# Kernel optimization log

Hardware: AMD Instinct MI355X
Metric: run time of the kernel (lower is better)

## Reference

```python
import jax, jax.numpy as jnp
import numpy as np

CIN = 128
COUT = 128
B = 8192
N_DIAG = 17
LENS = [9 - abs(i - 8) for i in range(N_DIAG)]  # [1,2,...,9,...,2,1]


def setup_inputs() -> dict:
    key = jax.random.key(0)
    ks = jax.random.split(key, 2 + N_DIAG)
    d = {
        "weights": jax.random.normal(ks[0], (N_DIAG, COUT, CIN), jnp.float32),
        "bias": jax.random.normal(ks[1], (N_DIAG, COUT), jnp.float32),
    }
    for i, L in enumerate(LENS):
        d[f"x{i}"] = jax.random.normal(ks[2 + i], (B, L, CIN), jnp.float32)
    return d


def _diag_idx(i):
    # board positions (r, c) on anti-diagonal r + c == i of a 9x9 board
    rs = np.arange(max(0, i - 8), min(8, i) + 1)
    cs = i - rs
    return rs, cs


def _forward(weights, bias, xs):
    b = xs[0].shape[0]
    out = jnp.zeros((b, 9, 9, weights.shape[1]), xs[0].dtype)
    for i, x in enumerate(xs):
        # per-diagonal linear transform: (B, L_i, Cin) @ (Cout, Cin)^T + bias
        y = jnp.einsum('blc,oc->blo', x, weights[i]) + bias[i]
        rs, cs = _diag_idx(i)  # static numpy indices -> jit-friendly scatter
        out = out.at[:, rs, cs, :].set(y)
    return out


def reference(weights, bias, x0, x1, x2, x3, x4, x5, x6, x7, x8, x9, x10, x11,
              x12, x13, x14, x15, x16):
    xs = (x0, x1, x2, x3, x4, x5, x6, x7, x8, x9, x10, x11, x12, x13, x14,
          x15, x16)
    return _forward(weights, bias, xs)
```

## Files before the change

kernel.cpp:

```cpp
#include <hip/hip_runtime.h>
#include <hip/hip_bf16.h>

typedef __attribute__((ext_vector_type(8))) short short8;
typedef __attribute__((ext_vector_type(4))) float f32x4;
typedef __attribute__((ext_vector_type(4))) unsigned int u32x4;

struct XPtrs { const float* p[17]; };
struct Bases { int v[18]; };

#define CPB 5

__device__ __forceinline__ unsigned short f2bf(float f) {
  unsigned u = __float_as_uint(f);
  return (unsigned short)((u + 0x7fffu + ((u >> 16) & 1u)) >> 16);
}

__global__ __launch_bounds__(1024) void convert_w_kernel(
    const float* __restrict__ W, unsigned short* __restrict__ ws) {
  const int tid = blockIdx.x * 1024 + threadIdx.x;
  const int d  = tid >> 11;
  const int s2 = tid & 2047;
  const int sg = s2 >> 7;
  const int n  = s2 & 127;
  const float* src = W + ((size_t)d * 128 + n) * 128 + sg * 8;
  float4 a = *(const float4*)(src);
  float4 b = *(const float4*)(src + 4);
  unsigned u0 = (unsigned)f2bf(a.x) | ((unsigned)f2bf(a.y) << 16);
  unsigned u1 = (unsigned)f2bf(a.z) | ((unsigned)f2bf(a.w) << 16);
  unsigned u2 = (unsigned)f2bf(b.x) | ((unsigned)f2bf(b.y) << 16);
  unsigned u3 = (unsigned)f2bf(b.z) | ((unsigned)f2bf(b.w) << 16);
  *(uint4*)(ws + (size_t)tid * 8) = make_uint4(u0, u1, u2, u3);
}

__device__ __forceinline__ unsigned pack_bf2(float lo, float hi) {
  unsigned rl = __float_as_uint(lo) + 0x8000u;
  unsigned rh = __float_as_uint(hi) + 0x8000u;
  return __builtin_amdgcn_perm(rh, rl, 0x07060302u);
}

__global__ __launch_bounds__(256) void diag_linear_kernel(
    XPtrs xp, Bases bb, const unsigned short* __restrict__ wsrc,
    const float* __restrict__ bias, float* __restrict__ out) {
  const int bid = blockIdx.x;
  int d = 0;
#pragma unroll
  for (int i = 1; i < 17; ++i) d += (bid >= bb.v[i]) ? 1 : 0;
  const int L = 9 - ((d < 8) ? (8 - d) : (d - 8));
  const int start = (d > 8) ? (d - 8) : 0;
  const float* __restrict__ x = xp.p[d];
  const int nunits = 128 * L;
  const int u0 = (bid - bb.v[d]) * CPB;
  const int nit = min(CPB, nunits - u0);

  const int t = threadIdx.x;
  const int lane = t & 63;
  const int wave = t >> 6;
  const int lr = lane & 15;
  const int lg = lane >> 4;

  __shared__ unsigned short wlds[2048 * 8];
  __shared__ float blds[128];

  {
    const unsigned short* gw = wsrc + (size_t)d * 16384;
    typedef const __attribute__((address_space(1))) unsigned int* gas_u32;
    typedef __attribute__((address_space(3))) unsigned int* las_u32;
#pragma unroll
    for (int r = 0; r < 8; ++r) {
      const int slotbase = (wave * 8 + r) * 64;
      __builtin_amdgcn_global_load_lds(
          (gas_u32)(const void*)(gw + (size_t)(slotbase + lane) * 8),
          (las_u32)(void*)(wlds + (size_t)slotbase * 8),
          16, 0, 0);
    }
    if (t < 32) {
      __builtin_amdgcn_global_load_lds(
          (gas_u32)(const void*)(bias + d * 128 + t * 4),
          (las_u32)(void*)(blds), 16, 0, 0);
    }
  }

  float4 pf[8];
  {
    const float* xr = x + ((size_t)(u0 * 64 + wave * 16 + lr)) * 128 + lg * 8;
#pragma unroll
    for (int s = 0; s < 4; ++s) {
      pf[2 * s]     = *(const float4*)(xr + s * 32);
      pf[2 * s + 1] = *(const float4*)(xr + s * 32 + 4);
    }
  }

  __syncthreads();

  for (int it = 0; it < nit; ++it) {
    const int u = u0 + it;

    short8 xf[4];
#pragma unroll
    for (int s = 0; s < 4; ++s) {
      float4 a0 = pf[2 * s], a1 = pf[2 * s + 1];
      u32x4 w;
      w.x = pack_bf2(a0.x, a0.y);
      w.y = pack_bf2(a0.z, a0.w);
      w.z = pack_bf2(a1.x, a1.y);
      w.w = pack_bf2(a1.z, a1.w);
      xf[s] = __builtin_bit_cast(short8, w);
    }

    {
      const int un = (it + 1 < nit) ? (u + 1) : u;
      const float* xr =
          x + ((size_t)(un * 64 + wave * 16 + lr)) * 128 + lg * 8;
#pragma unroll
      for (int s = 0; s < 4; ++s) {
        pf[2 * s]     = *(const float4*)(xr + s * 32);
        pf[2 * s + 1] = *(const float4*)(xr + s * 32 + 4);
      }
    }

    f32x4 acc[8];
#pragma unroll
    for (int nb = 0; nb < 8; ++nb)
      acc[nb] = *(const f32x4*)&blds[nb * 16 + lg * 4];

#pragma unroll
    for (int s = 0; s < 4; ++s) {
#pragma unroll
      for (int nb = 0; nb < 8; ++nb) {
        short8 wf = *(const short8*)
            &wlds[(size_t)((s * 4 + lg) * 128 + nb * 16 + lr) * 8];
        acc[nb] = __builtin_amdgcn_mfma_f32_16x16x32_bf16(wf, xf[s], acc[nb], 0, 0, 0);
      }
    }

    const int f = u * 64 + wave * 16 + lr;
    const unsigned b = (unsigned)f / (unsigned)L;
    const int l = f - (int)b * L;
    float* orow = out + (size_t)b * 10368 + (size_t)(start * 8 + d) * 128
                  + (size_t)l * 1024 + lg * 4;
#pragma unroll
    for (int nb = 0; nb < 8; ++nb)
      *(f32x4*)(orow + nb * 16) = acc[nb];
  }
}

extern "C" void kernel_launch(void* const* d_in, const int* in_sizes, int n_in,
                              void* d_out, int out_size, void* d_ws, size_t ws_size,
                              hipStream_t stream) {
  const float* W = (const float*)d_in[0];
  const float* bias = (const float*)d_in[1];
  XPtrs xp;
  for (int i = 0; i < 17; ++i) xp.p[i] = (const float*)d_in[2 + i];
  float* out = (float*)d_out;
  unsigned short* ws = (unsigned short*)d_ws;

  Bases bb;
  int base = 0;
  for (int i = 0; i < 17; ++i) {
    bb.v[i] = base;
    int L = 9 - ((i < 8) ? (8 - i) : (i - 8));
    base += (128 * L + CPB - 1) / CPB;
  }
  bb.v[17] = base;

  convert_w_kernel<<<34, 1024, 0, stream>>>(W, ws);
  diag_linear_kernel<<<base, 256, 0, stream>>>(xp, bb, ws, bias, out);
}
```

Before: 155.6 us.

## Double-buffer input prefetch two units ahead and raise units per block to eight

```diff
diff --git a/kernel.cpp b/kernel.cpp
--- a/kernel.cpp
+++ b/kernel.cpp
@@ -8,7 +8,7 @@
 struct XPtrs { const float* p[17]; };
 struct Bases { int v[18]; };
 
-#define CPB 5
+#define CPB 8
 
 __device__ __forceinline__ unsigned short f2bf(float f) {
   unsigned u = __float_as_uint(f);
@@ -38,6 +38,31 @@
   return __builtin_amdgcn_perm(rh, rl, 0x07060302u);
 }
 
+__device__ __forceinline__ void issue_unit_loads(
+    const float* __restrict__ x, int u, int wave, int lr, int lg,
+    float4 (&pf)[8]) {
+  const float* xr = x + ((size_t)(u * 64 + wave * 16 + lr)) * 128 + lg * 8;
+#pragma unroll
+  for (int s = 0; s < 4; ++s) {
+    pf[2 * s]     = *(const float4*)(xr + s * 32);
+    pf[2 * s + 1] = *(const float4*)(xr + s * 32 + 4);
+  }
+}
+
+__device__ __forceinline__ void convert_unit(const float4 (&pf)[8],
+                                             short8 (&xf)[4]) {
+#pragma unroll
+  for (int s = 0; s < 4; ++s) {
+    float4 a0 = pf[2 * s], a1 = pf[2 * s + 1];
+    u32x4 w;
+    w.x = pack_bf2(a0.x, a0.y);
+    w.y = pack_bf2(a0.z, a0.w);
+    w.z = pack_bf2(a1.x, a1.y);
+    w.w = pack_bf2(a1.z, a1.w);
+    xf[s] = __builtin_bit_cast(short8, w);
+  }
+}
+
 __global__ __launch_bounds__(256) void diag_linear_kernel(
     XPtrs xp, Bases bb, const unsigned short* __restrict__ wsrc,
     const float* __restrict__ bias, float* __restrict__ out) {
@@ -48,9 +73,7 @@
   const int L = 9 - ((d < 8) ? (8 - d) : (d - 8));
   const int start = (d > 8) ? (d - 8) : 0;
   const float* __restrict__ x = xp.p[d];
-  const int nunits = 128 * L;
   const int u0 = (bid - bb.v[d]) * CPB;
-  const int nit = min(CPB, nunits - u0);
 
   const int t = threadIdx.x;
   const int lane = t & 63;
@@ -80,67 +103,52 @@
     }
   }
 
-  float4 pf[8];
-  {
-    const float* xr = x + ((size_t)(u0 * 64 + wave * 16 + lr)) * 128 + lg * 8;
-#pragma unroll
-    for (int s = 0; s < 4; ++s) {
-      pf[2 * s]     = *(const float4*)(xr + s * 32);
-      pf[2 * s + 1] = *(const float4*)(xr + s * 32 + 4);
-    }
-  }
+  float4 pA[8], pB[8];
+  issue_unit_loads(x, u0,     wave, lr, lg, pA);
+  issue_unit_loads(x, u0 + 1, wave, lr, lg, pB);
 
   __syncthreads();
 
-  for (int it = 0; it < nit; ++it) {
-    const int u = u0 + it;
+  const int npair = CPB / 2;
+#pragma unroll
+  for (int k = 0; k < npair; ++k) {
+#pragma unroll
+    for (int ph = 0; ph < 2; ++ph) {
+      const int u = u0 + 2 * k + ph;
 
-    short8 xf[4];
+      short8 xf[4];
+      if (ph == 0) convert_unit(pA, xf);
+      else         convert_unit(pB, xf);
+
+      if (k + 1 < npair) {
+        if (ph == 0) issue_unit_loads(x, u + 2, wave, lr, lg, pA);
+        else         issue_unit_loads(x, u + 2, wave, lr, lg, pB);
+      }
+
+      f32x4 acc[8];
 #pragma unroll
-    for (int s = 0; s < 4; ++s) {
-      float4 a0 = pf[2 * s], a1 = pf[2 * s + 1];
-      u32x4 w;
-      w.x = pack_bf2(a0.x, a0.y);
-      w.y = pack_bf2(a0.z, a0.w);
-      w.z = pack_bf2(a1.x, a1.y);
-      w.w = pack_bf2(a1.z, a1.w);
-      xf[s] = __builtin_bit_cast(short8, w);
-    }
+      for (int nb = 0; nb < 8; ++nb)
+        acc[nb] = *(const f32x4*)&blds[nb * 16 + lg * 4];
 
-    {
-      const int un = (it + 1 < nit) ? (u + 1) : u;
-      const float* xr =
-          x + ((size_t)(un * 64 + wave * 16 + lr)) * 128 + lg * 8;
 #pragma unroll
       for (int s = 0; s < 4; ++s) {
-        pf[2 * s]     = *(const float4*)(xr + s * 32);
-        pf[2 * s + 1] = *(const float4*)(xr + s * 32 + 4);
+#pragma unroll
+        for (int nb = 0; nb < 8; ++nb) {
+          short8 wf = *(const short8*)
+              &wlds[(size_t)((s * 4 + lg) * 128 + nb * 16 + lr) * 8];
+          acc[nb] = __builtin_amdgcn_mfma_f32_16x16x32_bf16(wf, xf[s], acc[nb], 0, 0, 0);
+        }
       }
+
+      const int f = u * 64 + wave * 16 + lr;
+      const unsigned b = (unsigned)f / (unsigned)L;
+      const int l = f - (int)b * L;
+      float* orow = out + (size_t)b * 10368 + (size_t)(start * 8 + d) * 128
+                    + (size_t)l * 1024 + lg * 4;
+#pragma unroll
+      for (int nb = 0; nb < 8; ++nb)
+        *(f32x4*)(orow + nb * 16) = acc[nb];
     }
-
-    f32x4 acc[8];
-#pragma unroll
-    for (int nb = 0; nb < 8; ++nb)
-      acc[nb] = *(const f32x4*)&blds[nb * 16 + lg * 4];
-
-#pragma unroll
-    for (int s = 0; s < 4; ++s) {
-#pragma unroll
-      for (int nb = 0; nb < 8; ++nb) {
-        short8 wf = *(const short8*)
-            &wlds[(size_t)((s * 4 + lg) * 128 + nb * 16 + lr) * 8];
-        acc[nb] = __builtin_amdgcn_mfma_f32_16x16x32_bf16(wf, xf[s], acc[nb], 0, 0, 0);
-      }
-    }
-
-    const int f = u * 64 + wave * 16 + lr;
-    const unsigned b = (unsigned)f / (unsigned)L;
-    const int l = f - (int)b * L;
-    float* orow = out + (size_t)b * 10368 + (size_t)(start * 8 + d) * 128
-                  + (size_t)l * 1024 + lg * 4;
-#pragma unroll
-    for (int nb = 0; nb < 8; ++nb)
-      *(f32x4*)(orow + nb * 16) = acc[nb];
   }
 }
 
@@ -159,7 +167,7 @@
   for (int i = 0; i < 17; ++i) {
     bb.v[i] = base;
     int L = 9 - ((i < 8) ? (8 - i) : (i - 8));
-    base += (128 * L + CPB - 1) / CPB;
+    base += (128 * L) / CPB;
   }
   bb.v[17] = base;
 
```

Result: slower. 161.1 us (+3.6%).
